# Kernel optimization log

Hardware: AMD Instinct MI355X
Metric: run time of the kernel (lower is better)

Reference implementation:

```python
import jax, jax.numpy as jnp
import numpy as np

N_NODES = 50000
N_EDGES = 800000
IN_DIM = 64
HID = 128
N_LAYERS = 3
NEG_SLOPE = 0.2  # PyG GATConv default


def setup_inputs() -> dict:
    key = jax.random.key(0)
    ks = jax.random.split(key, 24)

    def lin(kw, kb, fan_in, fan_out):
        bound = 1.0 / np.sqrt(fan_in)
        W = jax.random.uniform(kw, (fan_out, fan_in), jnp.float32, -bound, bound)
        b = jax.random.uniform(kb, (fan_out,), jnp.float32, -bound, bound)
        return W, b

    x = jax.random.normal(ks[0], (N_NODES, IN_DIM), jnp.float32)
    h = jax.random.normal(ks[1], (N_NODES, HID), jnp.float32)
    edge_index = jax.random.randint(ks[2], (2, N_EDGES), 0, N_NODES, jnp.int64)

    W_enc, b_enc = lin(ks[3], ks[4], IN_DIM + HID, HID)

    # GAT layer params, stacked over layers: W [L,H,H], att vectors [L,H], bias [L,H]
    Wg = jnp.stack([lin(ks[5 + i], ks[8 + i], HID, HID)[0] for i in range(N_LAYERS)])
    att_src = jax.random.normal(ks[11], (N_LAYERS, HID), jnp.float32) * (1.0 / np.sqrt(HID))
    att_dst = jax.random.normal(ks[12], (N_LAYERS, HID), jnp.float32) * (1.0 / np.sqrt(HID))
    bg = jnp.zeros((N_LAYERS, HID), jnp.float32)

    Wd, bd = lin(ks[13], ks[14], 2 * HID, HID)
    Wd1, bd1 = lin(ks[15], ks[16], HID, HID)
    Wh, bh = lin(ks[17], ks[18], HID, 1)
    Wt, bt = lin(ks[19], ks[20], HID, 1)

    return dict(x=x, h=h, edge_index=edge_index, W_enc=W_enc, b_enc=b_enc,
                Wg=Wg, att_src=att_src, att_dst=att_dst, bg=bg,
                Wd=Wd, bd=bd, Wd1=Wd1, bd1=bd1, Wh=Wh, bh=bh, Wt=Wt, bt=bt)


def _gat_conv(xf, src, dst, W, a_s, a_d, b, n_nodes):
    # xf: [N,H]; messages flow src -> dst, softmax over incoming edges of dst
    xw = xf @ W.T                                   # [N,H]
    e = jax.nn.leaky_relu((xw @ a_s)[src] + (xw @ a_d)[dst], NEG_SLOPE)  # [E]
    m = jax.ops.segment_max(e, dst, num_segments=n_nodes)
    ex = jnp.exp(e - m[dst])
    denom = jax.ops.segment_sum(ex, dst, num_segments=n_nodes)
    alpha = ex / denom[dst]                         # [E]
    out = jax.ops.segment_sum(xw[src] * alpha[:, None], dst, num_segments=n_nodes)
    return out + b


def reference(x, h, edge_index, W_enc, b_enc, Wg, att_src, att_dst, bg,
              Wd, bd, Wd1, bd1, Wh, bh, Wt, bt):
    n = x.shape[0]
    # Encoder
    z = jnp.concatenate([x, h], axis=1) @ W_enc.T + b_enc   # [N,H]

    # add self-loops (PyG GATConv default add_self_loops=True)
    loops = jnp.arange(n, dtype=edge_index.dtype)
    src = jnp.concatenate([edge_index[0], loops])
    dst = jnp.concatenate([edge_index[1], loops])

    # GAT processor: relu(conv_i) for all layers, then last conv applied again (no relu)
    out = z
    for i in range(Wg.shape[0]):
        out = jax.nn.relu(_gat_conv(out, src, dst, Wg[i], att_src[i], att_dst[i], bg[i], n))
    hL = _gat_conv(out, src, dst, Wg[-1], att_src[-1], att_dst[-1], bg[-1], n)

    # Decoder (BatchNorm1d is defined but unused in the original forward)
    d = jax.nn.relu(jnp.concatenate([hL, z], axis=1) @ Wd.T + bd)
    d = jax.nn.relu(d @ Wd1.T + bd1)
    y = jax.nn.sigmoid(d @ Wh.T + bh)                        # [N,1]

    # Termination
    h_bar = jnp.mean(hL, axis=0)                             # [H]
    t = jax.nn.sigmoid(h_bar @ Wt.T + bt)                    # [1]
    return (y, t, hL)
```

## Files before the change

### kernel.cpp

```cpp
#include <hip/hip_runtime.h>

#define N_NODES 50000
#define N_EDGES 800000
#define E_TOT   (N_EDGES + N_NODES)
#define HID     128

typedef unsigned short u16;
typedef unsigned int   u32;
typedef __bf16 bf16x8 __attribute__((ext_vector_type(8)));
typedef float  f32x4  __attribute__((ext_vector_type(4)));

__device__ __forceinline__ float b2f(u16 u) {
  union { u32 i; float f; } c; c.i = ((u32)u) << 16; return c.f;
}
__device__ __forceinline__ u16 f2b(float f) {
  union { float f; u32 i; } c; c.f = f;
  u32 u = c.i;
  return (u16)((u + 0x7fffu + ((u >> 16) & 1u)) >> 16);
}


__global__ void k_detect(const void* x, const void* ei, int* flags) {
  int lane = threadIdx.x;
  const u16* xw = (const u16*)x;
  int wildF = 0;
  #pragma unroll
  for (int i = 0; i < 4; ++i) {
    u16 w = xw[lane + 64 * i];
    int e = (w >> 7) & 0xff;
    if (e >= 0x89) wildF = 1;
  }
  unsigned long long bF = __ballot(wildF);
  const int* e32 = (const int*)ei;
  int nzOdd = 0;
  #pragma unroll
  for (int i = 0; i < 2; ++i)
    if (e32[2 * (lane + 64 * i) + 1] != 0) nzOdd = 1;
  unsigned long long bI = __ballot(nzOdd);
  if (lane == 0) {
    flags[0] = (bF != 0ull) ? 1 : 0;
    flags[1] = (bI != 0ull) ? 0 : 1;
  }
}


__global__ __launch_bounds__(256) void k_convert(
    const void* Wenc, const void* Wg, const void* Wd, const void* Wd1,
    const void* benc, const void* bg, const void* atts, const void* attd,
    const void* bd, const void* bd1, const void* Wh, const void* bh,
    const void* Wt, const void* bt,
    u16* WencH, u16* WencL, u16* WgH, u16* WgL, u16* WdH, u16* WdL,
    u16* Wd1H, u16* Wd1L, float* vecf, const int* flags)
{
  int isF32 = flags[0];
  int t = blockIdx.x * 256 + threadIdx.x;
  auto ld = [&](const void* p, int i) -> float {
    return isF32 ? ((const float*)p)[i] : b2f(((const u16*)p)[i]);
  };
  auto sp = [&](u16* H, u16* L, int i, float v) {
    u16 hh = f2b(v); H[i] = hh; L[i] = f2b(v - b2f(hh));
  };
  if      (t < 24576)  { sp(WencH, WencL, t, ld(Wenc, t)); }
  else if (t < 73728)  { int i = t - 24576;  sp(WgH,  WgL,  i, ld(Wg, i)); }
  else if (t < 106496) { int i = t - 73728;  sp(WdH,  WdL,  i, ld(Wd, i)); }
  else if (t < 122880) { int i = t - 106496; sp(Wd1H, Wd1L, i, ld(Wd1, i)); }
  else if (t < 123008) { int i = t - 122880; vecf[i]        = ld(benc, i); }
  else if (t < 123392) { int i = t - 123008; vecf[128 + i]  = ld(bg, i); }
  else if (t < 123776) { int i = t - 123392; vecf[512 + i]  = ld(atts, i); }
  else if (t < 124160) { int i = t - 123776; vecf[896 + i]  = ld(attd, i); }
  else if (t < 124288) { int i = t - 124160; vecf[1280 + i] = ld(bd, i); }
  else if (t < 124416) { int i = t - 124288; vecf[1408 + i] = ld(bd1, i); }
  else if (t < 124544) { int i = t - 124416; vecf[1536 + i] = ld(Wh, i); }
  else if (t == 124544) { vecf[1664] = ld(bh, 0); }
  else if (t < 124673) { int i = t - 124545; vecf[1665 + i] = ld(Wt, i); }
  else if (t == 124673) { vecf[1793] = ld(bt, 0); }
}


__device__ __forceinline__ int ld_ei(const int* ei, size_t idx, int i64) {
  int v = i64 ? (int)((const long long*)ei)[idx] : ei[idx];
  return ((unsigned)v < (unsigned)N_NODES) ? v : 0;
}

__global__ void k_deg(const int* __restrict__ ei, int* __restrict__ deg, const int* flags) {
  int i64 = flags[1];
  int k = blockIdx.x * 256 + threadIdx.x;
  if (k >= E_TOT) return;
  int d = (k < N_EDGES) ? ld_ei(ei, (size_t)N_EDGES + k, i64) : (k - N_EDGES);
  atomicAdd(&deg[d], 1);
}

__device__ __forceinline__ int block_scan_excl(int v, int lane, int w, int* wsum, int& total) {
  int x = v;
  #pragma unroll
  for (int d = 1; d < 64; d <<= 1) {
    int y = __shfl_up(x, d);
    if (lane >= d) x += y;
  }
  if (lane == 63) wsum[w] = x;
  __syncthreads();
  int wOff = 0;
  #pragma unroll
  for (int i = 0; i < 4; ++i) wOff += (i < w) ? wsum[i] : 0;
  total = wsum[0] + wsum[1] + wsum[2] + wsum[3];
  return wOff + x - v;
}

__global__ void k_scan_block(const int* __restrict__ in, int* __restrict__ outExcl,
                             int* __restrict__ blkSum, int n, int* __restrict__ totalOut) {
  __shared__ int wsum[4];
  int t = threadIdx.x, lane = t & 63, w = t >> 6;
  int gid = blockIdx.x * 256 + t;
  int v = (gid < n) ? in[gid] : 0;
  int total;
  int excl = block_scan_excl(v, lane, w, wsum, total);
  if (gid < n) outExcl[gid] = excl;
  if (t == 0) {
    if (blkSum)   blkSum[blockIdx.x] = total;
    if (totalOut) totalOut[0] = total;
  }
}

__global__ void k_scan_add(int* __restrict__ rowp, const int* __restrict__ blkOff,
                           int* __restrict__ cursor, int n) {
  int gid = blockIdx.x * 256 + threadIdx.x;
  if (gid < n) {
    int r = rowp[gid] + blkOff[blockIdx.x];
    rowp[gid] = r;
    cursor[gid] = r;
  }
}

__global__ void k_scatter(const int* __restrict__ ei, int* __restrict__ cursor,
                          int* __restrict__ colsrc, const int* flags) {
  int i64 = flags[1];
  int k = blockIdx.x * 256 + threadIdx.x;
  if (k >= E_TOT) return;
  int s, d;
  if (k < N_EDGES) { s = ld_ei(ei, k, i64); d = ld_ei(ei, (size_t)N_EDGES + k, i64); }
  else             { s = d = k - N_EDGES; }
  int pos = atomicAdd(&cursor[d], 1);
  colsrc[pos] = s;
}


__device__ __forceinline__ void loadSplit8(const float* p, bf16x8& hi, bf16x8& lo) {
  union { u16 a[8]; bf16x8 v; } H, L;
  #pragma unroll
  for (int i = 0; i < 8; ++i) {
    float v = p[i];
    u16 hh = f2b(v);
    H.a[i] = hh;
    L.a[i] = f2b(v - b2f(hh));
  }
  hi = H.v; lo = L.v;
}

__global__ __launch_bounds__(256) void k_gemm(
    const void* A1a, const void* A1b, int s1, int K1,
    const void* A2a, const void* A2b, int s2,
    const u16* __restrict__ WH, const u16* __restrict__ WL,
    const float* __restrict__ biasF,
    float* __restrict__ outF_, u16* __restrict__ outH, u16* __restrict__ outL,
    const float* __restrict__ asv, const float* __restrict__ adv,
    float* __restrict__ ssrc, float* __restrict__ sdst,
    int N, int K, int relu, int aMode, const int* flags)
{
  int isF32 = flags[0];
  int wid  = blockIdx.x * 4 + (threadIdx.x >> 6);
  int lane = threadIdx.x & 63;
  int q = lane >> 4, c = lane & 15;
  int nb = wid * 32;
  if (nb >= N) return;
  f32x4 acc[2][8] = {};
  int r0 = nb + c;      if (r0 > N - 1) r0 = N - 1;
  int r1 = nb + 16 + c; if (r1 > N - 1) r1 = N - 1;

  for (int kb = 0; kb < K; kb += 32) {
    int kf = kb + q * 8;
    bf16x8 a0h, a1h, a0l, a1l;
    if (aMode == 1) {
      const void* Ap; int stride, ks;
      if (kf < K1) { Ap = A1a; stride = s1; ks = kf; }
      else         { Ap = A2a; stride = s2; ks = kf - K1; }
      if (isF32) {
        loadSplit8((const float*)Ap + (size_t)r0 * stride + ks, a0h, a0l);
        loadSplit8((const float*)Ap + (size_t)r1 * stride + ks, a1h, a1l);
      } else {
        union { u16 u[8]; bf16x8 v; } Z = {};
        a0h = *(const bf16x8*)((const u16*)Ap + (size_t)r0 * stride + ks);
        a1h = *(const bf16x8*)((const u16*)Ap + (size_t)r1 * stride + ks);
        a0l = Z.v; a1l = Z.v;
      }
    } else {
      const u16 *PH, *PL; int stride, ks;
      if (kf < K1) { PH = (const u16*)A1a; PL = (const u16*)A1b; stride = s1; ks = kf; }
      else         { PH = (const u16*)A2a; PL = (const u16*)A2b; stride = s2; ks = kf - K1; }
      a0h = *(const bf16x8*)(PH + (size_t)r0 * stride + ks);
      a0l = *(const bf16x8*)(PL + (size_t)r0 * stride + ks);
      a1h = *(const bf16x8*)(PH + (size_t)r1 * stride + ks);
      a1l = *(const bf16x8*)(PL + (size_t)r1 * stride + ks);
    }
    const u16* wph = WH + (size_t)c * K + kb + q * 8;
    const u16* wpl = WL + (size_t)c * K + kb + q * 8;
    #pragma unroll
    for (int ct = 0; ct < 8; ++ct) {
      bf16x8 bh_ = *(const bf16x8*)(wph + (size_t)(ct * 16) * K);
      bf16x8 bl_ = *(const bf16x8*)(wpl + (size_t)(ct * 16) * K);
      acc[0][ct] = __builtin_amdgcn_mfma_f32_16x16x32_bf16(a0h, bh_, acc[0][ct], 0, 0, 0);
      acc[1][ct] = __builtin_amdgcn_mfma_f32_16x16x32_bf16(a1h, bh_, acc[1][ct], 0, 0, 0);
      acc[0][ct] = __builtin_amdgcn_mfma_f32_16x16x32_bf16(a0h, bl_, acc[0][ct], 0, 0, 0);
      acc[1][ct] = __builtin_amdgcn_mfma_f32_16x16x32_bf16(a1h, bl_, acc[1][ct], 0, 0, 0);
      acc[0][ct] = __builtin_amdgcn_mfma_f32_16x16x32_bf16(a0l, bh_, acc[0][ct], 0, 0, 0);
      acc[1][ct] = __builtin_amdgcn_mfma_f32_16x16x32_bf16(a1l, bh_, acc[1][ct], 0, 0, 0);
    }
  }

  #pragma unroll
  for (int ct = 0; ct < 8; ++ct) {
    int col = ct * 16 + c;
    float bv = biasF ? biasF[col] : 0.0f;
    #pragma unroll
    for (int g = 0; g < 2; ++g) {
      #pragma unroll
      for (int r = 0; r < 4; ++r) {
        float vv = acc[g][ct][r] + bv;
        if (relu) vv = fmaxf(vv, 0.0f);
        acc[g][ct][r] = vv;
        int node = nb + g * 16 + q * 4 + r;
        if (node < N) {
          size_t o = (size_t)node * HID + col;
          if (outF_) outF_[o] = vv;
          if (outH) {
            u16 hh = f2b(vv);
            outH[o] = hh;
            outL[o] = f2b(vv - b2f(hh));
          }
        }
      }
    }
  }

  if (asv) {
    #pragma unroll
    for (int g = 0; g < 2; ++g) {
      #pragma unroll
      for (int r = 0; r < 4; ++r) {
        float ssum = 0.0f, dsum = 0.0f;
        #pragma unroll
        for (int ct = 0; ct < 8; ++ct) {
          int col = ct * 16 + c;
          float v = acc[g][ct][r];
          ssum += v * asv[col];
          dsum += v * adv[col];
        }
        #pragma unroll
        for (int m = 1; m < 16; m <<= 1) {
          ssum += __shfl_xor(ssum, m);
          dsum += __shfl_xor(dsum, m);
        }
        int node = nb + g * 16 + q * 4 + r;
        if (c == 0 && node < N) { ssrc[node] = ssum; sdst[node] = dsum; }
      }
    }
  }
}


__global__ __launch_bounds__(256) void k_fused(const int* __restrict__ rowp,
    const int* __restrict__ colsrc, const float* __restrict__ ssrc,
    const float* __restrict__ sdst, const float* __restrict__ xw,
    const float* __restrict__ biasF,
    u16* __restrict__ outH, u16* __restrict__ outL,
    float* __restrict__ out2, int relu)
{
  int node = blockIdx.x * 4 + (threadIdx.x >> 6);
  int lane = threadIdx.x & 63;
  int half = lane >> 5, hl = lane & 31;
  int start = rowp[node], end = rowp[node + 1];
  float sdv = sdst[node];

  int jC = start + lane;
  bool okC = jC < end;
  int   sC = okC ? colsrc[jC] : 0;
  float eC = -1e30f;
  if (okC) {
    float e = ssrc[sC] + sdv;
    eC = (e >= 0.0f) ? e : 0.2f * e;
  }
  float mx = eC;
  for (int j = start + 64 + lane; j < end; j += 64) {
    float e = ssrc[colsrc[j]] + sdv;
    e = (e >= 0.0f) ? e : 0.2f * e;
    mx = fmaxf(mx, e);
  }
  #pragma unroll
  for (int d = 1; d < 64; d <<= 1) mx = fmaxf(mx, __shfl_xor(mx, d));

  float sum = okC ? __expf(eC - mx) : 0.0f;
  for (int j = start + 64 + lane; j < end; j += 64) {
    float e = ssrc[colsrc[j]] + sdv;
    e = (e >= 0.0f) ? e : 0.2f * e;
    sum += __expf(e - mx);
  }
  #pragma unroll
  for (int d = 1; d < 64; d <<= 1) sum += __shfl_xor(sum, d);
  float inv = 1.0f / sum;
  float alC = okC ? __expf(eC - mx) * inv : 0.0f;

  float a0 = 0, a1 = 0, a2 = 0, a3 = 0;
  for (int j0 = start; j0 < end; j0 += 8) {
    int base = j0 - start;
    int   sI; float aI;
    if (base < 64) {
      sI = sC; aI = alC;
    } else {
      int idx = j0 + (lane & 7);
      bool ok = idx < end;
      sI = ok ? colsrc[idx] : 0;
      float e = ok ? (ssrc[sI] + sdv) : 0.0f;
      e = (e >= 0.0f) ? e : 0.2f * e;
      aI = ok ? __expf(e - mx) * inv : 0.0f;
    }
    int src = (base < 64) ? base : 0;
    #pragma unroll
    for (int t = 0; t < 8; t += 2) {
      int   ss = __shfl(sI, src + t + half);
      float aa = __shfl(aI, src + t + half);
      float4 p = *(const float4*)(xw + (size_t)ss * HID + hl * 4);
      a0 += aa * p.x; a1 += aa * p.y; a2 += aa * p.z; a3 += aa * p.w;
    }
  }
  a0 += __shfl_xor(a0, 32); a1 += __shfl_xor(a1, 32);
  a2 += __shfl_xor(a2, 32); a3 += __shfl_xor(a3, 32);
  if (half == 0) {
    int col = hl * 4;
    float4 b = *(const float4*)(biasF + col);
    a0 += b.x; a1 += b.y; a2 += b.z; a3 += b.w;
    if (relu) { a0 = fmaxf(a0, 0.f); a1 = fmaxf(a1, 0.f); a2 = fmaxf(a2, 0.f); a3 = fmaxf(a3, 0.f); }
    size_t o = (size_t)node * HID + col;
    u16 h0 = f2b(a0), h1 = f2b(a1), h2 = f2b(a2), h3 = f2b(a3);
    ushort4 hv; hv.x = h0; hv.y = h1; hv.z = h2; hv.w = h3;
    *(ushort4*)(outH + o) = hv;
    ushort4 lv;
    lv.x = f2b(a0 - b2f(h0)); lv.y = f2b(a1 - b2f(h1));
    lv.z = f2b(a2 - b2f(h2)); lv.w = f2b(a3 - b2f(h3));
    *(ushort4*)(outL + o) = lv;
    if (out2) { out2[o] = a0; out2[o + 1] = a1; out2[o + 2] = a2; out2[o + 3] = a3; }
  }
}


__global__ __launch_bounds__(256) void k_hbar(const u16* __restrict__ hH, const u16* __restrict__ hLo,
                                              float* __restrict__ hbar) {
  int t = threadIdx.x;
  int col = t & 127, g = t >> 7;
  float acc = 0.0f;
  for (int n = blockIdx.x * 2 + g; n < N_NODES; n += gridDim.x * 2) {
    size_t o = (size_t)n * HID + col;
    acc += b2f(hH[o]) + b2f(hLo[o]);
  }
  atomicAdd(&hbar[col], acc);
}


__global__ __launch_bounds__(256) void k_ydot(const float* __restrict__ d2,
    const float* __restrict__ Whf, const float* __restrict__ bhf, float* __restrict__ yout)
{
  int node = blockIdx.x * 4 + (threadIdx.x >> 6);
  int lane = threadIdx.x & 63;
  float2 p = *(const float2*)(d2 + (size_t)node * HID + lane * 2);
  float v = p.x * Whf[lane * 2] + p.y * Whf[lane * 2 + 1];
  #pragma unroll
  for (int d = 1; d < 64; d <<= 1) v += __shfl_xor(v, d);
  if (lane == 0) {
    float s = 1.0f / (1.0f + __expf(-(v + bhf[0])));
    yout[node] = s;
  }
}


__global__ void k_tker(const float* __restrict__ hbar, const float* __restrict__ Wtf,
                       const float* __restrict__ btf, float* __restrict__ tout) {
  int lane = threadIdx.x;
  float v = hbar[lane] * Wtf[lane] + hbar[lane + 64] * Wtf[lane + 64];
  #pragma unroll
  for (int d = 1; d < 64; d <<= 1) v += __shfl_xor(v, d);
  if (lane == 0) {
    float t = 1.0f / (1.0f + __expf(-(v * (1.0f / N_NODES) + btf[0])));
    tout[0] = t;
  }
}


extern "C" void kernel_launch(void* const* d_in, const int* in_sizes, int n_in,
                              void* d_out, int out_size, void* d_ws, size_t ws_size,
                              hipStream_t stream) {
  const void* x    = d_in[0];
  const void* h    = d_in[1];
  const int*  ei   = (const int*)d_in[2];
  const void* Wenc = d_in[3];
  const void* benc = d_in[4];
  const void* Wg   = d_in[5];
  const void* atts = d_in[6];
  const void* attd = d_in[7];
  const void* bg   = d_in[8];
  const void* Wd   = d_in[9];
  const void* bd   = d_in[10];
  const void* Wd1  = d_in[11];
  const void* bd1v = d_in[12];
  const void* Wh   = d_in[13];
  const void* bh   = d_in[14];
  const void* Wt   = d_in[15];
  const void* bt   = d_in[16];
  float* outF = (float*)d_out;

  char* w = (char*)d_ws;
  auto alloc = [&](size_t bytes) { char* p = w; w += (bytes + 255) & ~(size_t)255; return p; };
  const size_t NPLANE = (size_t)N_NODES * HID;
  float* xwF    = (float*)alloc(NPLANE * 4);
  u16*   zH     = (u16*)  alloc(NPLANE * 2);
  u16*   zL     = (u16*)  alloc(NPLANE * 2);
  u16*   aH     = (u16*)  alloc(NPLANE * 2);
  u16*   aL     = (u16*)  alloc(NPLANE * 2);
  float* ssrc   = (float*)alloc((size_t)N_NODES * 4);
  float* sdst   = (float*)alloc((size_t)N_NODES * 4);
  int*   deg    = (int*)  alloc((size_t)N_NODES * 4);
  int*   rowp   = (int*)  alloc((size_t)(N_NODES + 1) * 4);
  int*   cursor = (int*)  alloc((size_t)N_NODES * 4);
  int*   colsrc = (int*)  alloc((size_t)E_TOT * 4);
  int*   blkSum = (int*)  alloc(1024);
  int*   blkOff = (int*)  alloc(1024);
  float* hbar   = (float*)alloc(512);
  int*   flags  = (int*)  alloc(256);
  u16*   WencH  = (u16*)  alloc(24576 * 2);
  u16*   WencL  = (u16*)  alloc(24576 * 2);
  u16*   WgH    = (u16*)  alloc(49152 * 2);
  u16*   WgL    = (u16*)  alloc(49152 * 2);
  u16*   WdH    = (u16*)  alloc(32768 * 2);
  u16*   WdL    = (u16*)  alloc(32768 * 2);
  u16*   Wd1H   = (u16*)  alloc(16384 * 2);
  u16*   Wd1L   = (u16*)  alloc(16384 * 2);
  float* vecf   = (float*)alloc(2048 * 4);
  u16*   dH     = (u16*)xwF;
  u16*   dL     = dH + NPLANE;
  float* d2F    = (float*)aH;

  const int NODE_BLKS = N_NODES / 4;
  const int EDGE_BLKS = (E_TOT + 255) / 256;
  const int SCAN_BLKS = (N_NODES + 255) / 256;
  const int GEMM_BLKS = ((N_NODES + 31) / 32 + 3) / 4;
  const int CONV_BLKS = (124674 + 255) / 256;

  k_detect<<<1, 64, 0, stream>>>(x, ei, flags);
  k_convert<<<CONV_BLKS, 256, 0, stream>>>(Wenc, Wg, Wd, Wd1, benc, bg, atts, attd,
                                           bd, bd1v, Wh, bh, Wt, bt,
                                           WencH, WencL, WgH, WgL, WdH, WdL,
                                           Wd1H, Wd1L, vecf, flags);

  hipMemsetAsync(deg, 0, (size_t)N_NODES * 4, stream);
  hipMemsetAsync(hbar, 0, 128 * sizeof(float), stream);
  k_deg<<<EDGE_BLKS, 256, 0, stream>>>(ei, deg, flags);
  k_scan_block<<<SCAN_BLKS, 256, 0, stream>>>(deg, rowp, blkSum, N_NODES, nullptr);
  k_scan_block<<<1, 256, 0, stream>>>(blkSum, blkOff, nullptr, SCAN_BLKS, rowp + N_NODES);
  k_scan_add<<<SCAN_BLKS, 256, 0, stream>>>(rowp, blkOff, cursor, N_NODES);
  k_scatter<<<EDGE_BLKS, 256, 0, stream>>>(ei, cursor, colsrc, flags);

  k_gemm<<<GEMM_BLKS, 256, 0, stream>>>(x, nullptr, 64, 64, h, nullptr, HID,
                                        WencH, WencL, vecf,
                                        nullptr, zH, zL,
                                        nullptr, nullptr, nullptr, nullptr,
                                        N_NODES, 192, 0, 1, flags);

  for (int l4 = 0; l4 < 4; ++l4) {
    int l = (l4 < 3) ? l4 : 2;
    int relu = (l4 < 3) ? 1 : 0;
    const u16* inH = (l4 == 0) ? zH : aH;
    const u16* inL = (l4 == 0) ? zL : aL;
    k_gemm<<<GEMM_BLKS, 256, 0, stream>>>(inH, inL, HID, HID, nullptr, nullptr, HID,
                                          WgH + (size_t)l * HID * HID, WgL + (size_t)l * HID * HID,
                                          nullptr,
                                          xwF, nullptr, nullptr,
                                          vecf + 512 + l * HID, vecf + 896 + l * HID, ssrc, sdst,
                                          N_NODES, HID, 0, 2, flags);
    k_fused<<<NODE_BLKS, 256, 0, stream>>>(rowp, colsrc, ssrc, sdst, xwF, vecf + 128 + l * HID,
                                           aH, aL, (l4 == 3) ? (outF + N_NODES + 1) : nullptr, relu);
  }

  k_hbar<<<256, 256, 0, stream>>>(aH, aL, hbar);

  k_gemm<<<GEMM_BLKS, 256, 0, stream>>>(aH, aL, HID, HID, zH, zL, HID,
                                        WdH, WdL, vecf + 1280,
                                        nullptr, dH, dL,
                                        nullptr, nullptr, nullptr, nullptr,
                                        N_NODES, 256, 1, 2, flags);
  k_gemm<<<GEMM_BLKS, 256, 0, stream>>>(dH, dL, HID, HID, nullptr, nullptr, HID,
                                        Wd1H, Wd1L, vecf + 1408,
                                        d2F, nullptr, nullptr,
                                        nullptr, nullptr, nullptr, nullptr,
                                        N_NODES, 128, 1, 2, flags);
  k_ydot<<<NODE_BLKS, 256, 0, stream>>>(d2F, vecf + 1536, vecf + 1664, outF);
  k_tker<<<1, 64, 0, stream>>>(hbar, vecf + 1665, vecf + 1793, outF + N_NODES);
}
```

Baseline: 720.5 us.

## Split GAT aggregation into alpha pass and column-sliced gather over sliced xw layout

Changes the GEMM's fp32 xw output to a column-sliced layout (8 slices of 16 floats per node). The fused softmax+aggregate kernel is split in two: k_alpha writes (src, alpha) pairs per edge, and k_aggr runs one block per node group per slice, gathering 64-byte rows. The aim is better cache locality for the random neighbour gathers, since each slice's working set is smaller. It also folds the final y dot-product and sigmoid into the last decoder GEMM and uses nontemporal loads and stores. In exchange it adds a pairs buffer write and read per layer and re-reads the pairs once per slice.

```diff
diff --git a/kernel.cpp b/kernel.cpp
--- a/kernel.cpp
+++ b/kernel.cpp
@@ -4,11 +4,13 @@
 #define N_EDGES 800000
 #define E_TOT   (N_EDGES + N_NODES)
 #define HID     128
+#define NSLICE  8
 
 typedef unsigned short u16;
 typedef unsigned int   u32;
 typedef __bf16 bf16x8 __attribute__((ext_vector_type(8)));
 typedef float  f32x4  __attribute__((ext_vector_type(4)));
+typedef unsigned short u16x4 __attribute__((ext_vector_type(4)));
 
 __device__ __forceinline__ float b2f(u16 u) {
   union { u32 i; float f; } c; c.i = ((u32)u) << 16; return c.f;
@@ -164,6 +166,7 @@
     float* __restrict__ outF_, u16* __restrict__ outH, u16* __restrict__ outL,
     const float* __restrict__ asv, const float* __restrict__ adv,
     float* __restrict__ ssrc, float* __restrict__ sdst,
+    const float* __restrict__ yv, const float* __restrict__ ybp, float* __restrict__ yout,
     int N, int K, int relu, int aMode, const int* flags)
 {
   int isF32 = flags[0];
@@ -229,9 +232,9 @@
         acc[g][ct][r] = vv;
         int node = nb + g * 16 + q * 4 + r;
         if (node < N) {
-          size_t o = (size_t)node * HID + col;
-          if (outF_) outF_[o] = vv;
+          if (outF_) outF_[((size_t)ct * N + node) * 16 + c] = vv;
           if (outH) {
+            size_t o = (size_t)node * HID + col;
             u16 hh = f2b(vv);
             outH[o] = hh;
             outL[o] = f2b(vv - b2f(hh));
@@ -264,19 +267,32 @@
       }
     }
   }
-}
-
-
-__global__ __launch_bounds__(256) void k_fused(const int* __restrict__ rowp,
+
+  if (yv) {
+    #pragma unroll
+    for (int g = 0; g < 2; ++g) {
+      #pragma unroll
+      for (int r = 0; r < 4; ++r) {
+        float ssum = 0.0f;
+        #pragma unroll
+        for (int ct = 0; ct < 8; ++ct) ssum += acc[g][ct][r] * yv[ct * 16 + c];
+        #pragma unroll
+        for (int m = 1; m < 16; m <<= 1) ssum += __shfl_xor(ssum, m);
+        int node = nb + g * 16 + q * 4 + r;
+        if (c == 0 && node < N)
+          yout[node] = 1.0f / (1.0f + __expf(-(ssum + ybp[0])));
+      }
+    }
+  }
+}
+
+
+__global__ __launch_bounds__(256) void k_alpha(const int* __restrict__ rowp,
     const int* __restrict__ colsrc, const float* __restrict__ ssrc,
-    const float* __restrict__ sdst, const float* __restrict__ xw,
-    const float* __restrict__ biasF,
-    u16* __restrict__ outH, u16* __restrict__ outL,
-    float* __restrict__ out2, int relu)
+    const float* __restrict__ sdst, int2* __restrict__ pairs)
 {
   int node = blockIdx.x * 4 + (threadIdx.x >> 6);
   int lane = threadIdx.x & 63;
-  int half = lane >> 5, hl = lane & 31;
   int start = rowp[node], end = rowp[node + 1];
   float sdv = sdst[node];
 
@@ -306,47 +322,68 @@
   #pragma unroll
   for (int d = 1; d < 64; d <<= 1) sum += __shfl_xor(sum, d);
   float inv = 1.0f / sum;
-  float alC = okC ? __expf(eC - mx) * inv : 0.0f;
-
-  float a0 = 0, a1 = 0, a2 = 0, a3 = 0;
-  for (int j0 = start; j0 < end; j0 += 8) {
-    int base = j0 - start;
-    int   sI; float aI;
-    if (base < 64) {
-      sI = sC; aI = alC;
-    } else {
-      int idx = j0 + (lane & 7);
-      bool ok = idx < end;
-      sI = ok ? colsrc[idx] : 0;
-      float e = ok ? (ssrc[sI] + sdv) : 0.0f;
-      e = (e >= 0.0f) ? e : 0.2f * e;
-      aI = ok ? __expf(e - mx) * inv : 0.0f;
-    }
-    int src = (base < 64) ? base : 0;
-    #pragma unroll
-    for (int t = 0; t < 8; t += 2) {
-      int   ss = __shfl(sI, src + t + half);
-      float aa = __shfl(aI, src + t + half);
-      float4 p = *(const float4*)(xw + (size_t)ss * HID + hl * 4);
-      a0 += aa * p.x; a1 += aa * p.y; a2 += aa * p.z; a3 += aa * p.w;
-    }
-  }
-  a0 += __shfl_xor(a0, 32); a1 += __shfl_xor(a1, 32);
-  a2 += __shfl_xor(a2, 32); a3 += __shfl_xor(a3, 32);
-  if (half == 0) {
-    int col = hl * 4;
+
+  if (okC) {
+    int2 p; p.x = sC; p.y = __float_as_int(__expf(eC - mx) * inv);
+    pairs[jC] = p;
+  }
+  for (int j = start + 64 + lane; j < end; j += 64) {
+    int s = colsrc[j];
+    float e = ssrc[s] + sdv;
+    e = (e >= 0.0f) ? e : 0.2f * e;
+    int2 p; p.x = s; p.y = __float_as_int(__expf(e - mx) * inv);
+    pairs[j] = p;
+  }
+}
+
+
+__global__ __launch_bounds__(256) void k_aggr(const int* __restrict__ rowp,
+    const int2* __restrict__ pairs, const float* __restrict__ xwS,
+    const float* __restrict__ biasF,
+    u16* __restrict__ outH, u16* __restrict__ outL,
+    float* __restrict__ out2, int relu)
+{
+  int s    = blockIdx.x & 7;
+  int node = (blockIdx.x >> 3) * 4 + (threadIdx.x >> 6);
+  int lane = threadIdx.x & 63;
+  int e  = lane >> 2;
+  int c4 = lane & 3;
+  int start = rowp[node], end = rowp[node + 1];
+
+  const float* base = xwS + (size_t)s * ((size_t)N_NODES * 16) + c4 * 4;
+  float a0 = 0.f, a1 = 0.f, a2 = 0.f, a3 = 0.f;
+
+  for (int j0 = start; j0 < end; j0 += 16) {
+    int j = j0 + e;
+    long long pv = 0;
+    if (j < end) pv = __builtin_nontemporal_load((const long long*)pairs + j);
+    int   src = (int)(u32)pv;
+    float al  = __int_as_float((int)(pv >> 32));
+    float4 v = *(const float4*)(base + (size_t)src * 16);
+    a0 += al * v.x; a1 += al * v.y; a2 += al * v.z; a3 += al * v.w;
+  }
+  #pragma unroll
+  for (int m = 4; m < 64; m <<= 1) {
+    a0 += __shfl_xor(a0, m); a1 += __shfl_xor(a1, m);
+    a2 += __shfl_xor(a2, m); a3 += __shfl_xor(a3, m);
+  }
+  if (e == 0) {
+    int col = s * 16 + c4 * 4;
     float4 b = *(const float4*)(biasF + col);
     a0 += b.x; a1 += b.y; a2 += b.z; a3 += b.w;
     if (relu) { a0 = fmaxf(a0, 0.f); a1 = fmaxf(a1, 0.f); a2 = fmaxf(a2, 0.f); a3 = fmaxf(a3, 0.f); }
     size_t o = (size_t)node * HID + col;
     u16 h0 = f2b(a0), h1 = f2b(a1), h2 = f2b(a2), h3 = f2b(a3);
-    ushort4 hv; hv.x = h0; hv.y = h1; hv.z = h2; hv.w = h3;
-    *(ushort4*)(outH + o) = hv;
-    ushort4 lv;
+    u16x4 hv; hv.x = h0; hv.y = h1; hv.z = h2; hv.w = h3;
+    __builtin_nontemporal_store(hv, (u16x4*)(outH + o));
+    u16x4 lv;
     lv.x = f2b(a0 - b2f(h0)); lv.y = f2b(a1 - b2f(h1));
     lv.z = f2b(a2 - b2f(h2)); lv.w = f2b(a3 - b2f(h3));
-    *(ushort4*)(outL + o) = lv;
-    if (out2) { out2[o] = a0; out2[o + 1] = a1; out2[o + 2] = a2; out2[o + 3] = a3; }
+    __builtin_nontemporal_store(lv, (u16x4*)(outL + o));
+    if (out2) {
+      f32x4 fv; fv.x = a0; fv.y = a1; fv.z = a2; fv.w = a3;
+      __builtin_nontemporal_store(fv, (f32x4*)(out2 + o));
+    }
   }
 }
 
@@ -361,22 +398,6 @@
     acc += b2f(hH[o]) + b2f(hLo[o]);
   }
   atomicAdd(&hbar[col], acc);
-}
-
-
-__global__ __launch_bounds__(256) void k_ydot(const float* __restrict__ d2,
-    const float* __restrict__ Whf, const float* __restrict__ bhf, float* __restrict__ yout)
-{
-  int node = blockIdx.x * 4 + (threadIdx.x >> 6);
-  int lane = threadIdx.x & 63;
-  float2 p = *(const float2*)(d2 + (size_t)node * HID + lane * 2);
-  float v = p.x * Whf[lane * 2] + p.y * Whf[lane * 2 + 1];
-  #pragma unroll
-  for (int d = 1; d < 64; d <<= 1) v += __shfl_xor(v, d);
-  if (lane == 0) {
-    float s = 1.0f / (1.0f + __expf(-(v + bhf[0])));
-    yout[node] = s;
-  }
 }
 
 
@@ -418,7 +439,7 @@
   char* w = (char*)d_ws;
   auto alloc = [&](size_t bytes) { char* p = w; w += (bytes + 255) & ~(size_t)255; return p; };
   const size_t NPLANE = (size_t)N_NODES * HID;
-  float* xwF    = (float*)alloc(NPLANE * 4);
+  float* xwS    = (float*)alloc(NPLANE * 4);
   u16*   zH     = (u16*)  alloc(NPLANE * 2);
   u16*   zL     = (u16*)  alloc(NPLANE * 2);
   u16*   aH     = (u16*)  alloc(NPLANE * 2);
@@ -429,6 +450,7 @@
   int*   rowp   = (int*)  alloc((size_t)(N_NODES + 1) * 4);
   int*   cursor = (int*)  alloc((size_t)N_NODES * 4);
   int*   colsrc = (int*)  alloc((size_t)E_TOT * 4);
+  int2*  pairs  = (int2*) alloc((size_t)E_TOT * 8);
   int*   blkSum = (int*)  alloc(1024);
   int*   blkOff = (int*)  alloc(1024);
   float* hbar   = (float*)alloc(512);
@@ -442,11 +464,11 @@
   u16*   Wd1H   = (u16*)  alloc(16384 * 2);
   u16*   Wd1L   = (u16*)  alloc(16384 * 2);
   float* vecf   = (float*)alloc(2048 * 4);
-  u16*   dH     = (u16*)xwF;
+  u16*   dH     = (u16*)xwS;
   u16*   dL     = dH + NPLANE;
-  float* d2F    = (float*)aH;
 
   const int NODE_BLKS = N_NODES / 4;
+  const int AGGR_BLKS = NODE_BLKS * NSLICE;
   const int EDGE_BLKS = (E_TOT + 255) / 256;
   const int SCAN_BLKS = (N_NODES + 255) / 256;
   const int GEMM_BLKS = ((N_NODES + 31) / 32 + 3) / 4;
@@ -470,6 +492,7 @@
                                         WencH, WencL, vecf,
                                         nullptr, zH, zL,
                                         nullptr, nullptr, nullptr, nullptr,
+                                        nullptr, nullptr, nullptr,
                                         N_NODES, 192, 0, 1, flags);
 
   for (int l4 = 0; l4 < 4; ++l4) {
@@ -480,11 +503,13 @@
     k_gemm<<<GEMM_BLKS, 256, 0, stream>>>(inH, inL, HID, HID, nullptr, nullptr, HID,
                                           WgH + (size_t)l * HID * HID, WgL + (size_t)l * HID * HID,
                                           nullptr,
-                                          xwF, nullptr, nullptr,
+                                          xwS, nullptr, nullptr,
                                           vecf + 512 + l * HID, vecf + 896 + l * HID, ssrc, sdst,
+                                          nullptr, nullptr, nullptr,
                                           N_NODES, HID, 0, 2, flags);
-    k_fused<<<NODE_BLKS, 256, 0, stream>>>(rowp, colsrc, ssrc, sdst, xwF, vecf + 128 + l * HID,
-                                           aH, aL, (l4 == 3) ? (outF + N_NODES + 1) : nullptr, relu);
+    k_alpha<<<NODE_BLKS, 256, 0, stream>>>(rowp, colsrc, ssrc, sdst, pairs);
+    k_aggr<<<AGGR_BLKS, 256, 0, stream>>>(rowp, pairs, xwS, vecf + 128 + l * HID,
+                                          aH, aL, (l4 == 3) ? (outF + N_NODES + 1) : nullptr, relu);
   }
 
   k_hbar<<<256, 256, 0, stream>>>(aH, aL, hbar);
@@ -493,12 +518,13 @@
                                         WdH, WdL, vecf + 1280,
                                         nullptr, dH, dL,
                                         nullptr, nullptr, nullptr, nullptr,
+                                        nullptr, nullptr, nullptr,
                                         N_NODES, 256, 1, 2, flags);
   k_gemm<<<GEMM_BLKS, 256, 0, stream>>>(dH, dL, HID, HID, nullptr, nullptr, HID,
                                         Wd1H, Wd1L, vecf + 1408,
-                                        d2F, nullptr, nullptr,
+                                        nullptr, nullptr, nullptr,
                                         nullptr, nullptr, nullptr, nullptr,
+                                        vecf + 1536, vecf + 1664, outF,
                                         N_NODES, 128, 1, 2, flags);
-  k_ydot<<<NODE_BLKS, 256, 0, stream>>>(d2F, vecf + 1536, vecf + 1664, outF);
   k_tker<<<1, 64, 0, stream>>>(hbar, vecf + 1665, vecf + 1793, outF + N_NODES);
 }
```

After: 1.198 ms. 66.2% more time.
